# Kernel optimization log

Hardware: AMD Instinct MI355X
Metric: run time of the kernel (lower is better)

Reference implementation:

```python
import jax, jax.numpy as jnp
import numpy as np

B, C, N, T, H = 4, 128, 512, 16, 4
DK = C // H
SCALE = float(np.sqrt(DK) * 1.0)  # dk**0.5 * max(tau,1e-6), tau=1.0


def setup_inputs() -> dict:
    key = jax.random.key(0)
    ks = jax.random.split(key, 6)
    x = jax.random.normal(ks[0], (B, C, N, T), jnp.float32)
    Wq = jax.random.normal(ks[1], (C, C), jnp.float32) * (1.0 / np.sqrt(C))
    Wk = jax.random.normal(ks[2], (C, C), jnp.float32) * (1.0 / np.sqrt(C))
    # original init is identity; add tiny noise so it's not degenerate
    structural = jnp.eye(N, dtype=jnp.float32) + 0.01 * jax.random.normal(ks[3], (N, N), jnp.float32)
    fusion_w = jax.random.normal(ks[4], (2,), jnp.float32) * 0.5  # 1x1 conv over 2 input channels
    fusion_b = (jax.random.normal(ks[5], (), jnp.float32) * 0.1)
    return {"x": x, "Wq": Wq, "Wk": Wk, "structural": structural,
            "fusion_w": fusion_w, "fusion_b": fusion_b}


def reference(x, Wq, Wk, structural, fusion_w, fusion_b):
    # x: [B, C, N, T]. 1x1 conv == per-channel linear; arrange to [B,T,N,H,DK]
    Q = jnp.einsum('oc,bcnt->btno', Wq, x).reshape(B, T, N, H, DK)
    K = jnp.einsum('oc,bcnt->btno', Wk, x).reshape(B, T, N, H, DK)
    # scores: [B, T, H, N, N]
    scores = jnp.einsum('btnhd,btmhd->bthnm', Q, K) / SCALE
    att_node = jax.nn.softmax(scores, axis=-1).mean(axis=(1, 2))  # [B, N, N]
    att_struct = jax.nn.softmax(structural, axis=-1)              # [N, N]
    # fusion conv (1x1, 2->1 channels) == weighted sum + bias
    fused = fusion_w[0] * att_node + fusion_w[1] * att_struct[None] + fusion_b
    fused = 0.5 * (fused + jnp.swapaxes(fused, 1, 2))  # symmetrize
    fused = jax.nn.softmax(fused, axis=-1)             # normalize='softmax'
    x_bt = jnp.transpose(x, (0, 3, 2, 1))              # [B, T, N, C]
    x_att = jnp.einsum('bij,btjc->btic', fused, x_bt)  # weighted aggregation over nodes
    return jnp.transpose(x_att, (0, 3, 2, 1))          # [B, C, N, T]
```

## Files before the change

### kernel.cpp

```cpp
#include <hip/hip_runtime.h>

#define BB 4
#define CC 128
#define NN 512
#define TT 16
#define HH 4
#define DKK 32
#define GPART 8
#define INV_SCALE 0.17677669529663687f

typedef __attribute__((ext_vector_type(8))) short bf16x8;
typedef __attribute__((ext_vector_type(4))) float f32x4;

__device__ __forceinline__ unsigned int pk2bf(float a, float b) {
  unsigned int ua = __float_as_uint(a);
  ua = (ua + 0x7FFFu + ((ua >> 16) & 1u)) >> 16;
  unsigned int ub = __float_as_uint(b);
  ub = (ub + 0x7FFFu + ((ub >> 16) & 1u)) >> 16;
  return ua | (ub << 16);
}

__device__ __forceinline__ ushort cv1(float f) {
  unsigned int u = __float_as_uint(f);
  return (ushort)((u + 0x7FFFu + ((u >> 16) & 1u)) >> 16);
}

__device__ __forceinline__ unsigned int pkfast(float a, float b) {
  unsigned int au = __float_as_uint(a) + 0x8000u;
  unsigned int bu = __float_as_uint(b) + 0x8000u;
  return __builtin_amdgcn_perm(bu, au, 0x07060302u);
}

__device__ __forceinline__ float bf2f(ushort v) {
  return __uint_as_float((unsigned int)v << 16);
}

__global__ __launch_bounds__(256) void k_proj(const float* __restrict__ x,
                                              const float* __restrict__ Wq,
                                              const float* __restrict__ Wk,
                                              ushort* __restrict__ Qb,
                                              ushort* __restrict__ Kb) {
  __shared__ float xl[128 * 66];
  const int b = blockIdx.y;
  const int nt0 = blockIdx.x * 64;
  const int nq = nt0 >> 4;
  const int tid = threadIdx.x;
  const int w = tid >> 6, lane = tid & 63;
  const int lm = lane & 15, quad = lane >> 4;

  const float* xb = x + (size_t)b * 1048576 + nt0;
#pragma unroll
  for (int L = tid * 4; L < 8192; L += 1024) {
    int c = L >> 6, j = L & 63;
    float4 v = *(const float4*)(xb + c * 8192 + j);
    float2* dp = (float2*)(xl + c * 66 + j);
    dp[0] = make_float2(v.x, v.y);
    dp[1] = make_float2(v.z, v.w);
  }

  const int o0 = w * 32;
  bf16x8 aq[2][4], ak[2][4];
#pragma unroll
  for (int ot = 0; ot < 2; ++ot)
#pragma unroll
    for (int kc = 0; kc < 4; ++kc) {
      const int off = (o0 + ot * 16 + lm) * 128 + kc * 32 + quad * 8;
      const float4 q1 = *(const float4*)(Wq + off);
      const float4 q2 = *(const float4*)(Wq + off + 4);
      const float4 k1 = *(const float4*)(Wk + off);
      const float4 k2 = *(const float4*)(Wk + off + 4);
      union { uint4 u; bf16x8 v; } cq, ck;
      cq.u.x = pk2bf(q1.x * INV_SCALE, q1.y * INV_SCALE);
      cq.u.y = pk2bf(q1.z * INV_SCALE, q1.w * INV_SCALE);
      cq.u.z = pk2bf(q2.x * INV_SCALE, q2.y * INV_SCALE);
      cq.u.w = pk2bf(q2.z * INV_SCALE, q2.w * INV_SCALE);
      ck.u.x = pk2bf(k1.x, k1.y);
      ck.u.y = pk2bf(k1.z, k1.w);
      ck.u.z = pk2bf(k2.x, k2.y);
      ck.u.w = pk2bf(k2.z, k2.w);
      aq[ot][kc] = cq.v;
      ak[ot][kc] = ck.v;
    }
  __syncthreads();

#pragma unroll
  for (int jtl = 0; jtl < 4; ++jtl) {
    bf16x8 bfr[4];
#pragma unroll
    for (int kc = 0; kc < 4; ++kc) {
      const float* sp = xl + (kc * 32 + quad * 8) * 66 + jtl * 16 + lm;
      float f0 = sp[0],   f1 = sp[66],  f2 = sp[132], f3 = sp[198];
      float f4 = sp[264], f5 = sp[330], f6 = sp[396], f7 = sp[462];
      union { uint4 u; bf16x8 v; } cv;
      cv.u.x = pkfast(f0, f1);
      cv.u.y = pkfast(f2, f3);
      cv.u.z = pkfast(f4, f5);
      cv.u.w = pkfast(f6, f7);
      bfr[kc] = cv.v;
    }

    f32x4 accq0 = {0,0,0,0}, accq1 = {0,0,0,0};
    f32x4 acck0 = {0,0,0,0}, acck1 = {0,0,0,0};
#pragma unroll
    for (int kc = 0; kc < 4; ++kc) {
      accq0 = __builtin_amdgcn_mfma_f32_16x16x32_bf16(aq[0][kc], bfr[kc], accq0, 0, 0, 0);
      accq1 = __builtin_amdgcn_mfma_f32_16x16x32_bf16(aq[1][kc], bfr[kc], accq1, 0, 0, 0);
      acck0 = __builtin_amdgcn_mfma_f32_16x16x32_bf16(ak[0][kc], bfr[kc], acck0, 0, 0, 0);
      acck1 = __builtin_amdgcn_mfma_f32_16x16x32_bf16(ak[1][kc], bfr[kc], acck1, 0, 0, 0);
    }

    const size_t base = (size_t)b * 1048576 + (size_t)lm * 65536 + w * 16384 +
                        (size_t)(nq + jtl) * 32 + quad * 4;
    uint2 uq0, uq1, uk0, uk1;
    uq0.x = pk2bf(accq0[0], accq0[1]); uq0.y = pk2bf(accq0[2], accq0[3]);
    uq1.x = pk2bf(accq1[0], accq1[1]); uq1.y = pk2bf(accq1[2], accq1[3]);
    uk0.x = pk2bf(acck0[0], acck0[1]); uk0.y = pk2bf(acck0[2], acck0[3]);
    uk1.x = pk2bf(acck1[0], acck1[1]); uk1.y = pk2bf(acck1[2], acck1[3]);
    *(uint2*)(Qb + base)      = uq0;
    *(uint2*)(Qb + base + 16) = uq1;
    *(uint2*)(Kb + base)      = uk0;
    *(uint2*)(Kb + base + 16) = uk1;
  }
}

__global__ __launch_bounds__(256, 4) void k_scores(const ushort* __restrict__ Qb,
                                                   const ushort* __restrict__ Kb,
                                                   ushort* __restrict__ part) {
  __shared__ float SH[16 * 516];
  __shared__ float red[2][4][16];
  const int strip = blockIdx.x, g = blockIdx.y, b = blockIdx.z;
  const int tid = threadIdx.x;
  const int w = tid >> 6, lane = tid & 63;
  const int lm = lane & 15, quad = lane >> 4;
  const int n0 = strip * 16;
  const int wcol0 = w * 128;

  float acc[32];
#pragma unroll
  for (int i = 0; i < 32; ++i) acc[i] = 0.f;

  for (int pi = 0; pi < 8; ++pi) {
    const int p = (g << 3) + pi;
    const size_t base = (size_t)((b * 16 + (p >> 2)) * 4 + (p & 3)) * 16384;
    bf16x8 afrag = *(const bf16x8*)(Qb + base + (size_t)(n0 + lm) * 32 + quad * 8);
    bf16x8 bfr[8];
#pragma unroll
    for (int ct = 0; ct < 8; ++ct)
      bfr[ct] = *(const bf16x8*)(Kb + base + (size_t)(wcol0 + ct * 16 + lm) * 32 + quad * 8);

    f32x4 d[8];
#pragma unroll
    for (int ct = 0; ct < 8; ++ct) {
      f32x4 z = {0.f, 0.f, 0.f, 0.f};
      d[ct] = __builtin_amdgcn_mfma_f32_16x16x32_bf16(afrag, bfr[ct], z, 0, 0, 0);
    }

    float cur[32];
    float rp0 = 0.f, rp1 = 0.f, rp2 = 0.f, rp3 = 0.f;
#pragma unroll
    for (int ct = 0; ct < 8; ++ct) {
      float e0 = __expf(d[ct][0]);
      float e1 = __expf(d[ct][1]);
      float e2 = __expf(d[ct][2]);
      float e3 = __expf(d[ct][3]);
      cur[ct * 4 + 0] = e0; cur[ct * 4 + 1] = e1;
      cur[ct * 4 + 2] = e2; cur[ct * 4 + 3] = e3;
      rp0 += e0; rp1 += e1; rp2 += e2; rp3 += e3;
    }
#pragma unroll
    for (int m = 1; m < 16; m <<= 1) {
      rp0 += __shfl_xor(rp0, m);
      rp1 += __shfl_xor(rp1, m);
      rp2 += __shfl_xor(rp2, m);
      rp3 += __shfl_xor(rp3, m);
    }
    if (lm == 0) {
      red[pi & 1][w][quad * 4 + 0] = rp0;
      red[pi & 1][w][quad * 4 + 1] = rp1;
      red[pi & 1][w][quad * 4 + 2] = rp2;
      red[pi & 1][w][quad * 4 + 3] = rp3;
    }
    __syncthreads();
#pragma unroll
    for (int r = 0; r < 4; ++r) {
      float rs = red[pi & 1][0][quad * 4 + r] + red[pi & 1][1][quad * 4 + r] +
                 red[pi & 1][2][quad * 4 + r] + red[pi & 1][3][quad * 4 + r];
      float inv = 1.0f / rs;
#pragma unroll
      for (int ct = 0; ct < 8; ++ct)
        acc[ct * 4 + r] = fmaf(cur[ct * 4 + r], inv, acc[ct * 4 + r]);
    }
  }

#pragma unroll
  for (int ct = 0; ct < 8; ++ct) {
#pragma unroll
    for (int r = 0; r < 4; ++r)
      SH[(quad * 4 + r) * 516 + wcol0 + ct * 16 + lm] = acc[ct * 4 + r];
  }
  __syncthreads();
  const int row = tid >> 4, colb = (tid & 15) * 4;
  ushort* po = part + ((size_t)((g * 4 + b) * 512 + n0 + row)) * 512 + colb;
#pragma unroll
  for (int k = 0; k < 8; ++k) {
    f32x4 v = *(const f32x4*)(SH + row * 516 + colb + k * 64);
    uint2 u;
    u.x = pk2bf(v[0], v[1]);
    u.y = pk2bf(v[2], v[3]);
    *(uint2*)(po + k * 64) = u;
  }
}

__global__ __launch_bounds__(256) void k_xconv(const float* __restrict__ x,
                                               ushort* __restrict__ xtb) {
  __shared__ ushort xs[16 * 520];
  const int c = blockIdx.x, b = blockIdx.y;
  const int tid = threadIdx.x;
  const float* in = x + ((size_t)b * 128 + c) * 8192;
  ushort* outp = xtb + ((size_t)b * 128 + c) * 8192;

#pragma unroll
  for (int it = 0; it < 8; ++it) {
    int idx = (tid + it * 256) * 4;
    int j = idx >> 4, t0 = idx & 15;
    float4 v = *(const float4*)(in + idx);
    xs[(t0 + 0) * 520 + j] = cv1(v.x);
    xs[(t0 + 1) * 520 + j] = cv1(v.y);
    xs[(t0 + 2) * 520 + j] = cv1(v.z);
    xs[(t0 + 3) * 520 + j] = cv1(v.w);
  }
  __syncthreads();
#pragma unroll
  for (int it = 0; it < 4; ++it) {
    int u = (tid + it * 256) * 8;
    int t = u >> 9, j0 = u & 511;
    *(uint4*)(outp + u) = *(const uint4*)(xs + t * 520 + j0);
  }
}

__device__ __forceinline__ float blk_max(float v, float* red, int tid) {
#pragma unroll
  for (int off = 32; off > 0; off >>= 1) v = fmaxf(v, __shfl_xor(v, off, 64));
  if ((tid & 63) == 0) red[tid >> 6] = v;
  __syncthreads();
  v = fmaxf(fmaxf(red[0], red[1]), fmaxf(red[2], red[3]));
  __syncthreads();
  return v;
}
__device__ __forceinline__ float blk_sum(float v, float* red, int tid) {
#pragma unroll
  for (int off = 32; off > 0; off >>= 1) v += __shfl_xor(v, off, 64);
  if ((tid & 63) == 0) red[tid >> 6] = v;
  __syncthreads();
  v = (red[0] + red[1]) + (red[2] + red[3]);
  __syncthreads();
  return v;
}

__global__ __launch_bounds__(256) void k_struct(const float* __restrict__ S,
                                                float* __restrict__ st) {
  __shared__ float red[4];
  const int i = blockIdx.x, tid = threadIdx.x;
  float s0 = S[i * 512 + tid], s1 = S[i * 512 + tid + 256];
  float m = blk_max(fmaxf(s0, s1), red, tid);
  float e0 = __expf(s0 - m), e1 = __expf(s1 - m);
  float sum = blk_sum(e0 + e1, red, tid);
  float inv = 1.0f / sum;
  st[i * 512 + tid] = e0 * inv;
  st[i * 512 + tid + 256] = e1 * inv;
}

__global__ __launch_bounds__(256) void k_redsym(const ushort* __restrict__ part,
                                                float* __restrict__ Ssym,
                                                float* __restrict__ st) {
  __shared__ float L1[64 * 68];
  __shared__ float L2[64 * 68];
  const int z = blockIdx.y;
  int rem = blockIdx.x, ti = 0;
  for (;;) { int cnt = 8 - ti; if (rem < cnt) break; rem -= cnt; ++ti; }
  const int tj = ti + rem;
  const bool diag = (ti == tj);
  const int tid = threadIdx.x;
  const int rr = tid >> 2, cc = (tid & 3) * 16;

  float a1[16], a2[16];
#pragma unroll
  for (int k = 0; k < 16; ++k) { a1[k] = 0.f; a2[k] = 0.f; }

  if (z == 4) {
    const float* p1 = st + (ti * 64 + rr) * 512 + tj * 64 + cc;
    const float* p2 = st + (tj * 64 + rr) * 512 + ti * 64 + cc;
#pragma unroll
    for (int q = 0; q < 4; ++q) {
      float4 v = *(const float4*)(p1 + q * 4);
      a1[q * 4 + 0] = v.x; a1[q * 4 + 1] = v.y;
      a1[q * 4 + 2] = v.z; a1[q * 4 + 3] = v.w;
      if (!diag) {
        float4 u = *(const float4*)(p2 + q * 4);
        a2[q * 4 + 0] = u.x; a2[q * 4 + 1] = u.y;
        a2[q * 4 + 2] = u.z; a2[q * 4 + 3] = u.w;
      }
    }
  } else {
    const int b = z;
#pragma unroll
    for (int g = 0; g < GPART; ++g) {
      const ushort* p1 = part + ((size_t)((g * 4 + b) * 512 + ti * 64 + rr)) * 512 + tj * 64 + cc;
      const ushort* p2 = part + ((size_t)((g * 4 + b) * 512 + tj * 64 + rr)) * 512 + ti * 64 + cc;
#pragma unroll
      for (int q = 0; q < 4; ++q) {
        ushort4 v = *(const ushort4*)(p1 + q * 4);
        a1[q * 4 + 0] += bf2f(v.x); a1[q * 4 + 1] += bf2f(v.y);
        a1[q * 4 + 2] += bf2f(v.z); a1[q * 4 + 3] += bf2f(v.w);
        if (!diag) {
          ushort4 u = *(const ushort4*)(p2 + q * 4);
          a2[q * 4 + 0] += bf2f(u.x); a2[q * 4 + 1] += bf2f(u.y);
          a2[q * 4 + 2] += bf2f(u.z); a2[q * 4 + 3] += bf2f(u.w);
        }
      }
    }
  }

#pragma unroll
  for (int q = 0; q < 4; ++q) {
    *(float4*)(L1 + rr * 68 + cc + q * 4) =
        make_float4(a1[q * 4], a1[q * 4 + 1], a1[q * 4 + 2], a1[q * 4 + 3]);
    if (!diag)
      *(float4*)(L2 + rr * 68 + cc + q * 4) =
          make_float4(a2[q * 4], a2[q * 4 + 1], a2[q * 4 + 2], a2[q * 4 + 3]);
  }
  __syncthreads();

  float* M = (z < 4) ? (Ssym + (size_t)z * 262144) : st;
  const float* LT = diag ? L1 : L2;
#pragma unroll
  for (int q = 0; q < 4; ++q) {
    const int c = cc + q * 4;
    float4 o;
    o.x = L1[rr * 68 + c + 0] + LT[(c + 0) * 68 + rr];
    o.y = L1[rr * 68 + c + 1] + LT[(c + 1) * 68 + rr];
    o.z = L1[rr * 68 + c + 2] + LT[(c + 2) * 68 + rr];
    o.w = L1[rr * 68 + c + 3] + LT[(c + 3) * 68 + rr];
    *(float4*)(M + (ti * 64 + rr) * 512 + tj * 64 + c) = o;
  }
  if (!diag) {
#pragma unroll
    for (int q = 0; q < 4; ++q) {
      const int c = cc + q * 4;
      float4 o;
      o.x = L2[rr * 68 + c + 0] + L1[(c + 0) * 68 + rr];
      o.y = L2[rr * 68 + c + 1] + L1[(c + 1) * 68 + rr];
      o.z = L2[rr * 68 + c + 2] + L1[(c + 2) * 68 + rr];
      o.w = L2[rr * 68 + c + 3] + L1[(c + 3) * 68 + rr];
      *(float4*)(M + (tj * 64 + rr) * 512 + ti * 64 + c) = o;
    }
  }
}

__global__ __launch_bounds__(256) void k_fused(const float* __restrict__ Ssym,
                                               const float* __restrict__ st,
                                               const float* __restrict__ fw,
                                               const float* __restrict__ fb,
                                               ushort* __restrict__ fusedb) {
  __shared__ float red[4];
  const int i = blockIdx.x, b = blockIdx.y, tid = threadIdx.x;
  const float w0s = fw[0] * (0.5f / 64.f);
  const float w1s = fw[1] * 0.5f;
  const float bias = fb[0];
  const float* A = Ssym + (size_t)b * 262144 + (size_t)i * 512;
  const float* S = st + (size_t)i * 512;
  float2 a2 = *(const float2*)(A + tid * 2);
  float2 s2 = *(const float2*)(S + tid * 2);
  float l0 = fmaf(w0s, a2.x, fmaf(w1s, s2.x, bias));
  float l1 = fmaf(w0s, a2.y, fmaf(w1s, s2.y, bias));
  float m = blk_max(fmaxf(l0, l1), red, tid);
  float e0 = __expf(l0 - m), e1 = __expf(l1 - m);
  float sum = blk_sum(e0 + e1, red, tid);
  float inv = 1.0f / sum;
  *(unsigned int*)(fusedb + ((size_t)(b * 512 + i)) * 512 + tid * 2) =
      pk2bf(e0 * inv, e1 * inv);
}

__global__ __launch_bounds__(256) void k_agg(const ushort* __restrict__ fusedb,
                                             const ushort* __restrict__ xtb,
                                             float* __restrict__ out) {
  __shared__ ushort xs[16 * 520];
  const int cg = blockIdx.x;
  const int i0 = blockIdx.y * 64;
  const int b = blockIdx.z;
  const int tid = threadIdx.x, w = tid >> 6, lane = tid & 63;
  const int lm = lane & 15, quad = lane >> 4;

  const ushort* fr = fusedb + ((size_t)(b * 512 + i0 + w * 16 + lm)) * 512 + quad * 8;
  bf16x8 af[16];
#pragma unroll
  for (int kk = 0; kk < 16; ++kk) af[kk] = *(const bf16x8*)(fr + kk * 32);

  const ushort* xg = xtb + ((size_t)b * 128 + cg * 8) * 8192;
  uint4 rg[4];
#pragma unroll
  for (int it = 0; it < 4; ++it) rg[it] = *(const uint4*)(xg + (tid + it * 256) * 8);

  for (int c = 0; c < 8; ++c) {
#pragma unroll
    for (int it = 0; it < 4; ++it) {
      int u = (tid + it * 256) * 8;
      int t = u >> 9, j0 = u & 511;
      *(uint4*)(xs + t * 520 + j0) = rg[it];
    }
    __syncthreads();
    if (c < 7) {
      const ushort* xg2 = xg + (size_t)(c + 1) * 8192;
#pragma unroll
      for (int it = 0; it < 4; ++it) rg[it] = *(const uint4*)(xg2 + (tid + it * 256) * 8);
    }
    f32x4 acc = {0.f, 0.f, 0.f, 0.f};
#pragma unroll
    for (int kk = 0; kk < 16; ++kk) {
      bf16x8 bf = *(const bf16x8*)(xs + lm * 520 + kk * 32 + quad * 8);
      acc = __builtin_amdgcn_mfma_f32_16x16x32_bf16(af[kk], bf, acc, 0, 0, 0);
    }
    float* op = out + (size_t)b * 1048576 + (size_t)(cg * 8 + c) * 8192 +
                (size_t)(i0 + w * 16 + quad * 4) * 16 + lm;
    op[0]  = acc[0];
    op[16] = acc[1];
    op[32] = acc[2];
    op[48] = acc[3];
    __syncthreads();
  }
}

extern "C" void kernel_launch(void* const* d_in, const int* in_sizes, int n_in,
                              void* d_out, int out_size, void* d_ws, size_t ws_size,
                              hipStream_t stream) {
  const float* x  = (const float*)d_in[0];
  const float* Wq = (const float*)d_in[1];
  const float* Wk = (const float*)d_in[2];
  const float* S  = (const float*)d_in[3];
  const float* fw = (const float*)d_in[4];
  const float* fb = (const float*)d_in[5];
  float* out = (float*)d_out;

  ushort* Qb   = (ushort*)d_ws;
  ushort* Kb   = Qb + 4194304;
  ushort* part = Kb + 4194304;
  ushort* xtb  = part;
  float* Ssym  = (float*)(part + 8388608);
  float* st    = Ssym + 1048576;
  ushort* fusedb = (ushort*)(st + 262144);

  k_proj  <<<dim3(128, 4),      256, 0, stream>>>(x, Wq, Wk, Qb, Kb);
  k_scores<<<dim3(32, GPART, 4),256, 0, stream>>>(Qb, Kb, part);
  k_struct<<<dim3(512),         256, 0, stream>>>(S, st);
  k_redsym<<<dim3(36, 5),       256, 0, stream>>>(part, Ssym, st);
  k_xconv <<<dim3(128, 4),      256, 0, stream>>>(x, xtb);
  k_fused <<<dim3(512, 4),      256, 0, stream>>>(Ssym, st, fw, fb, fusedb);
  k_agg   <<<dim3(16, 8, 4),    256, 0, stream>>>(fusedb, xtb, out);
}
```

Before: 166.6 us.

## Fuse all stages into one cooperative persistent kernel with grid syncs

```diff
diff --git a/kernel.cpp b/kernel.cpp
--- a/kernel.cpp
+++ b/kernel.cpp
@@ -1,13 +1,11 @@
 #include <hip/hip_runtime.h>
-
-#define BB 4
-#define CC 128
-#define NN 512
-#define TT 16
-#define HH 4
-#define DKK 32
-#define GPART 8
+#include <hip/hip_cooperative_groups.h>
+
+namespace cg = cooperative_groups;
+
+#define GPART 4
 #define INV_SCALE 0.17677669529663687f
+#define SMEM_SZ 36864
 
 typedef __attribute__((ext_vector_type(8))) short bf16x8;
 typedef __attribute__((ext_vector_type(4))) float f32x4;
@@ -19,30 +17,24 @@
   ub = (ub + 0x7FFFu + ((ub >> 16) & 1u)) >> 16;
   return ua | (ub << 16);
 }
-
 __device__ __forceinline__ ushort cv1(float f) {
   unsigned int u = __float_as_uint(f);
   return (ushort)((u + 0x7FFFu + ((u >> 16) & 1u)) >> 16);
 }
-
 __device__ __forceinline__ unsigned int pkfast(float a, float b) {
   unsigned int au = __float_as_uint(a) + 0x8000u;
   unsigned int bu = __float_as_uint(b) + 0x8000u;
   return __builtin_amdgcn_perm(bu, au, 0x07060302u);
 }
-
 __device__ __forceinline__ float bf2f(ushort v) {
   return __uint_as_float((unsigned int)v << 16);
 }
 
-__global__ __launch_bounds__(256) void k_proj(const float* __restrict__ x,
-                                              const float* __restrict__ Wq,
-                                              const float* __restrict__ Wk,
-                                              ushort* __restrict__ Qb,
-                                              ushort* __restrict__ Kb) {
-  __shared__ float xl[128 * 66];
-  const int b = blockIdx.y;
-  const int nt0 = blockIdx.x * 64;
+__device__ void ph_proj(const float* x, const float* Wq, const float* Wk,
+                        ushort* Qb, ushort* Kb, char* smem, int bid) {
+  float* xl = (float*)smem;
+  const int b = bid >> 7;
+  const int nt0 = (bid & 127) * 64;
   const int nq = nt0 >> 4;
   const int tid = threadIdx.x;
   const int w = tid >> 6, lane = tid & 63;
@@ -123,12 +115,42 @@
   }
 }
 
-__global__ __launch_bounds__(256, 4) void k_scores(const ushort* __restrict__ Qb,
-                                                   const ushort* __restrict__ Kb,
-                                                   ushort* __restrict__ part) {
-  __shared__ float SH[16 * 516];
-  __shared__ float red[2][4][16];
-  const int strip = blockIdx.x, g = blockIdx.y, b = blockIdx.z;
+__device__ __forceinline__ float blk_max(float v, float* red, int tid) {
+#pragma unroll
+  for (int off = 32; off > 0; off >>= 1) v = fmaxf(v, __shfl_xor(v, off, 64));
+  if ((tid & 63) == 0) red[tid >> 6] = v;
+  __syncthreads();
+  v = fmaxf(fmaxf(red[0], red[1]), fmaxf(red[2], red[3]));
+  __syncthreads();
+  return v;
+}
+__device__ __forceinline__ float blk_sum(float v, float* red, int tid) {
+#pragma unroll
+  for (int off = 32; off > 0; off >>= 1) v += __shfl_xor(v, off, 64);
+  if ((tid & 63) == 0) red[tid >> 6] = v;
+  __syncthreads();
+  v = (red[0] + red[1]) + (red[2] + red[3]);
+  __syncthreads();
+  return v;
+}
+
+__device__ void ph_struct(const float* S, float* st, char* smem, int bid) {
+  float* red = (float*)(smem + 34816);
+  const int i = bid, tid = threadIdx.x;
+  float s0 = S[i * 512 + tid], s1 = S[i * 512 + tid + 256];
+  float m = blk_max(fmaxf(s0, s1), red, tid);
+  float e0 = __expf(s0 - m), e1 = __expf(s1 - m);
+  float sum = blk_sum(e0 + e1, red, tid);
+  float inv = 1.0f / sum;
+  st[i * 512 + tid] = e0 * inv;
+  st[i * 512 + tid + 256] = e1 * inv;
+}
+
+__device__ void ph_scores(const ushort* Qb, const ushort* Kb, ushort* part,
+                          char* smem, int bid) {
+  float* SH = (float*)smem;
+  float (*red)[4][16] = (float(*)[4][16])(smem + 33024);
+  const int strip = bid & 31, g = (bid >> 5) & 3, b = bid >> 7;
   const int tid = threadIdx.x;
   const int w = tid >> 6, lane = tid & 63;
   const int lm = lane & 15, quad = lane >> 4;
@@ -139,8 +161,8 @@
 #pragma unroll
   for (int i = 0; i < 32; ++i) acc[i] = 0.f;
 
-  for (int pi = 0; pi < 8; ++pi) {
-    const int p = (g << 3) + pi;
+  for (int pi = 0; pi < 16; ++pi) {
+    const int p = g * 16 + pi;
     const size_t base = (size_t)((b * 16 + (p >> 2)) * 4 + (p & 3)) * 16384;
     bf16x8 afrag = *(const bf16x8*)(Qb + base + (size_t)(n0 + lm) * 32 + quad * 8);
     bf16x8 bfr[8];
@@ -211,10 +233,9 @@
   }
 }
 
-__global__ __launch_bounds__(256) void k_xconv(const float* __restrict__ x,
-                                               ushort* __restrict__ xtb) {
-  __shared__ ushort xs[16 * 520];
-  const int c = blockIdx.x, b = blockIdx.y;
+__device__ void ph_xconv(const float* x, ushort* xtb, char* smem, int bid) {
+  ushort* xs = (ushort*)smem;
+  const int c = bid & 127, b = bid >> 7;
   const int tid = threadIdx.x;
   const float* in = x + ((size_t)b * 128 + c) * 8192;
   ushort* outp = xtb + ((size_t)b * 128 + c) * 8192;
@@ -238,45 +259,12 @@
   }
 }
 
-__device__ __forceinline__ float blk_max(float v, float* red, int tid) {
-#pragma unroll
-  for (int off = 32; off > 0; off >>= 1) v = fmaxf(v, __shfl_xor(v, off, 64));
-  if ((tid & 63) == 0) red[tid >> 6] = v;
-  __syncthreads();
-  v = fmaxf(fmaxf(red[0], red[1]), fmaxf(red[2], red[3]));
-  __syncthreads();
-  return v;
-}
-__device__ __forceinline__ float blk_sum(float v, float* red, int tid) {
-#pragma unroll
-  for (int off = 32; off > 0; off >>= 1) v += __shfl_xor(v, off, 64);
-  if ((tid & 63) == 0) red[tid >> 6] = v;
-  __syncthreads();
-  v = (red[0] + red[1]) + (red[2] + red[3]);
-  __syncthreads();
-  return v;
-}
-
-__global__ __launch_bounds__(256) void k_struct(const float* __restrict__ S,
-                                                float* __restrict__ st) {
-  __shared__ float red[4];
-  const int i = blockIdx.x, tid = threadIdx.x;
-  float s0 = S[i * 512 + tid], s1 = S[i * 512 + tid + 256];
-  float m = blk_max(fmaxf(s0, s1), red, tid);
-  float e0 = __expf(s0 - m), e1 = __expf(s1 - m);
-  float sum = blk_sum(e0 + e1, red, tid);
-  float inv = 1.0f / sum;
-  st[i * 512 + tid] = e0 * inv;
-  st[i * 512 + tid + 256] = e1 * inv;
-}
-
-__global__ __launch_bounds__(256) void k_redsym(const ushort* __restrict__ part,
-                                                float* __restrict__ Ssym,
-                                                float* __restrict__ st) {
-  __shared__ float L1[64 * 68];
-  __shared__ float L2[64 * 68];
-  const int z = blockIdx.y;
-  int rem = blockIdx.x, ti = 0;
+__device__ void ph_redsym(const ushort* part, float* Ssym, float* st,
+                          char* smem, int bid) {
+  float* L1 = (float*)smem;
+  float* L2 = L1 + 64 * 68;
+  const int z = bid / 36;
+  int rem = bid % 36, ti = 0;
   for (;;) { int cnt = 8 - ti; if (rem < cnt) break; rem -= cnt; ++ti; }
   const int tj = ti + rem;
   const bool diag = (ti == tj);
@@ -357,37 +345,35 @@
   }
 }
 
-__global__ __launch_bounds__(256) void k_fused(const float* __restrict__ Ssym,
-                                               const float* __restrict__ st,
-                                               const float* __restrict__ fw,
-                                               const float* __restrict__ fb,
-                                               ushort* __restrict__ fusedb) {
-  __shared__ float red[4];
-  const int i = blockIdx.x, b = blockIdx.y, tid = threadIdx.x;
+__device__ void ph_fused(const float* Ssym, const float* st, const float* fw,
+                         const float* fb, ushort* fusedb, char* smem, int bid) {
+  float* red = (float*)smem;
+  const int i = bid, tid = threadIdx.x;
   const float w0s = fw[0] * (0.5f / 64.f);
   const float w1s = fw[1] * 0.5f;
   const float bias = fb[0];
-  const float* A = Ssym + (size_t)b * 262144 + (size_t)i * 512;
   const float* S = st + (size_t)i * 512;
-  float2 a2 = *(const float2*)(A + tid * 2);
   float2 s2 = *(const float2*)(S + tid * 2);
-  float l0 = fmaf(w0s, a2.x, fmaf(w1s, s2.x, bias));
-  float l1 = fmaf(w0s, a2.y, fmaf(w1s, s2.y, bias));
-  float m = blk_max(fmaxf(l0, l1), red, tid);
-  float e0 = __expf(l0 - m), e1 = __expf(l1 - m);
-  float sum = blk_sum(e0 + e1, red, tid);
-  float inv = 1.0f / sum;
-  *(unsigned int*)(fusedb + ((size_t)(b * 512 + i)) * 512 + tid * 2) =
-      pk2bf(e0 * inv, e1 * inv);
-}
-
-__global__ __launch_bounds__(256) void k_agg(const ushort* __restrict__ fusedb,
-                                             const ushort* __restrict__ xtb,
-                                             float* __restrict__ out) {
-  __shared__ ushort xs[16 * 520];
-  const int cg = blockIdx.x;
-  const int i0 = blockIdx.y * 64;
-  const int b = blockIdx.z;
+  for (int b = 0; b < 4; ++b) {
+    const float* A = Ssym + (size_t)b * 262144 + (size_t)i * 512;
+    float2 a2 = *(const float2*)(A + tid * 2);
+    float l0 = fmaf(w0s, a2.x, fmaf(w1s, s2.x, bias));
+    float l1 = fmaf(w0s, a2.y, fmaf(w1s, s2.y, bias));
+    float m = blk_max(fmaxf(l0, l1), red, tid);
+    float e0 = __expf(l0 - m), e1 = __expf(l1 - m);
+    float sum = blk_sum(e0 + e1, red, tid);
+    float inv = 1.0f / sum;
+    *(unsigned int*)(fusedb + ((size_t)(b * 512 + i)) * 512 + tid * 2) =
+        pk2bf(e0 * inv, e1 * inv);
+  }
+}
+
+__device__ void ph_agg(const ushort* fusedb, const ushort* xtb, float* out,
+                       char* smem, int bid) {
+  ushort* xs = (ushort*)smem;
+  const int cg = bid & 15;
+  const int i0 = ((bid >> 4) & 7) * 64;
+  const int b = bid >> 7;
   const int tid = threadIdx.x, w = tid >> 6, lane = tid & 63;
   const int lm = lane & 15, quad = lane >> 4;
 
@@ -428,6 +414,63 @@
     op[48] = acc[3];
     __syncthreads();
   }
+}
+
+__global__ __launch_bounds__(256, 2) void k_mega(const float* x, const float* Wq,
+                                                 const float* Wk, const float* S,
+                                                 const float* fw, const float* fb,
+                                                 float* out, ushort* Qb, ushort* Kb,
+                                                 ushort* part, ushort* xtb,
+                                                 float* Ssym, float* st,
+                                                 ushort* fusedb) {
+  __shared__ __align__(16) char smem[SMEM_SZ];
+  const int bid = blockIdx.x;
+  cg::grid_group grid = cg::this_grid();
+
+  ph_proj(x, Wq, Wk, Qb, Kb, smem, bid);
+  ph_struct(S, st, smem, bid);
+  grid.sync();
+  ph_scores(Qb, Kb, part, smem, bid);
+  grid.sync();
+  ph_xconv(x, xtb, smem, bid);
+  __syncthreads();
+  if (bid < 180) ph_redsym(part, Ssym, st, smem, bid);
+  grid.sync();
+  ph_fused(Ssym, st, fw, fb, fusedb, smem, bid);
+  grid.sync();
+  ph_agg(fusedb, xtb, out, smem, bid);
+}
+
+__global__ __launch_bounds__(256, 2) void k_ph1(const float* x, const float* Wq,
+                                                const float* Wk, const float* S,
+                                                ushort* Qb, ushort* Kb, float* st) {
+  __shared__ __align__(16) char smem[SMEM_SZ];
+  ph_proj(x, Wq, Wk, Qb, Kb, smem, blockIdx.x);
+  ph_struct(S, st, smem, blockIdx.x);
+}
+__global__ __launch_bounds__(256, 2) void k_ph2(const ushort* Qb, const ushort* Kb,
+                                                ushort* part) {
+  __shared__ __align__(16) char smem[SMEM_SZ];
+  ph_scores(Qb, Kb, part, smem, blockIdx.x);
+}
+__global__ __launch_bounds__(256, 2) void k_ph3(const float* x, ushort* xtb,
+                                                const ushort* part, float* Ssym,
+                                                float* st) {
+  __shared__ __align__(16) char smem[SMEM_SZ];
+  ph_xconv(x, xtb, smem, blockIdx.x);
+  __syncthreads();
+  if (blockIdx.x < 180) ph_redsym(part, Ssym, st, smem, blockIdx.x);
+}
+__global__ __launch_bounds__(256, 2) void k_ph4(const float* Ssym, const float* st,
+                                                const float* fw, const float* fb,
+                                                ushort* fusedb) {
+  __shared__ __align__(16) char smem[SMEM_SZ];
+  ph_fused(Ssym, st, fw, fb, fusedb, smem, blockIdx.x);
+}
+__global__ __launch_bounds__(256, 2) void k_ph5(const ushort* fusedb,
+                                                const ushort* xtb, float* out) {
+  __shared__ __align__(16) char smem[SMEM_SZ];
+  ph_agg(fusedb, xtb, out, smem, blockIdx.x);
 }
 
 extern "C" void kernel_launch(void* const* d_in, const int* in_sizes, int n_in,
@@ -444,16 +487,21 @@
   ushort* Qb   = (ushort*)d_ws;
   ushort* Kb   = Qb + 4194304;
   ushort* part = Kb + 4194304;
-  ushort* xtb  = part;
-  float* Ssym  = (float*)(part + 8388608);
+  ushort* xtb  = Qb;
+  float* Ssym  = (float*)(part + 4194304);
   float* st    = Ssym + 1048576;
   ushort* fusedb = (ushort*)(st + 262144);
 
-  k_proj  <<<dim3(128, 4),      256, 0, stream>>>(x, Wq, Wk, Qb, Kb);
-  k_scores<<<dim3(32, GPART, 4),256, 0, stream>>>(Qb, Kb, part);
-  k_struct<<<dim3(512),         256, 0, stream>>>(S, st);
-  k_redsym<<<dim3(36, 5),       256, 0, stream>>>(part, Ssym, st);
-  k_xconv <<<dim3(128, 4),      256, 0, stream>>>(x, xtb);
-  k_fused <<<dim3(512, 4),      256, 0, stream>>>(Ssym, st, fw, fb, fusedb);
-  k_agg   <<<dim3(16, 8, 4),    256, 0, stream>>>(fusedb, xtb, out);
-}
+  void* args[] = {(void*)&x, (void*)&Wq, (void*)&Wk, (void*)&S, (void*)&fw,
+                  (void*)&fb, (void*)&out, (void*)&Qb, (void*)&Kb, (void*)&part,
+                  (void*)&xtb, (void*)&Ssym, (void*)&st, (void*)&fusedb};
+  hipError_t e = hipLaunchCooperativeKernel((const void*)k_mega, dim3(512),
+                                            dim3(256), args, 0, stream);
+  if (e != hipSuccess) {
+    k_ph1<<<dim3(512), 256, 0, stream>>>(x, Wq, Wk, S, Qb, Kb, st);
+    k_ph2<<<dim3(512), 256, 0, stream>>>(Qb, Kb, part);
+    k_ph3<<<dim3(512), 256, 0, stream>>>(x, xtb, part, Ssym, st);
+    k_ph4<<<dim3(512), 256, 0, stream>>>(Ssym, st, fw, fb, fusedb);
+    k_ph5<<<dim3(512), 256, 0, stream>>>(fusedb, xtb, out);
+  }
+}
```

Measured after the change: 424.0 us. 154% more time.

## Merge seven kernel launches into five by co-scheduling independent phases

Applied to the files above, without the earlier changes.

```diff
diff --git a/kernel.cpp b/kernel.cpp
--- a/kernel.cpp
+++ b/kernel.cpp
@@ -1,13 +1,8 @@
 #include <hip/hip_runtime.h>
 
-#define BB 4
-#define CC 128
-#define NN 512
-#define TT 16
-#define HH 4
-#define DKK 32
 #define GPART 8
 #define INV_SCALE 0.17677669529663687f
+#define SMEM_SZ 36864
 
 typedef __attribute__((ext_vector_type(8))) short bf16x8;
 typedef __attribute__((ext_vector_type(4))) float f32x4;
@@ -19,30 +14,50 @@
   ub = (ub + 0x7FFFu + ((ub >> 16) & 1u)) >> 16;
   return ua | (ub << 16);
 }
-
 __device__ __forceinline__ ushort cv1(float f) {
   unsigned int u = __float_as_uint(f);
   return (ushort)((u + 0x7FFFu + ((u >> 16) & 1u)) >> 16);
 }
-
 __device__ __forceinline__ unsigned int pkfast(float a, float b) {
   unsigned int au = __float_as_uint(a) + 0x8000u;
   unsigned int bu = __float_as_uint(b) + 0x8000u;
   return __builtin_amdgcn_perm(bu, au, 0x07060302u);
 }
-
 __device__ __forceinline__ float bf2f(ushort v) {
   return __uint_as_float((unsigned int)v << 16);
 }
 
-__global__ __launch_bounds__(256) void k_proj(const float* __restrict__ x,
-                                              const float* __restrict__ Wq,
-                                              const float* __restrict__ Wk,
-                                              ushort* __restrict__ Qb,
-                                              ushort* __restrict__ Kb) {
-  __shared__ float xl[128 * 66];
-  const int b = blockIdx.y;
-  const int nt0 = blockIdx.x * 64;
+__device__ __forceinline__ float blk_max(float v, float* red, int tid) {
+#pragma unroll
+  for (int off = 32; off > 0; off >>= 1) v = fmaxf(v, __shfl_xor(v, off, 64));
+  if ((tid & 63) == 0) red[tid >> 6] = v;
+  __syncthreads();
+  v = fmaxf(fmaxf(red[0], red[1]), fmaxf(red[2], red[3]));
+  __syncthreads();
+  return v;
+}
+__device__ __forceinline__ float blk_sum(float v, float* red, int tid) {
+#pragma unroll
+  for (int off = 32; off > 0; off >>= 1) v += __shfl_xor(v, off, 64);
+  if ((tid & 63) == 0) red[tid >> 6] = v;
+  __syncthreads();
+  v = (red[0] + red[1]) + (red[2] + red[3]);
+  __syncthreads();
+  return v;
+}
+
+__global__ __launch_bounds__(256) void k_ph1(const float* __restrict__ x,
+                                             const float* __restrict__ Wq,
+                                             const float* __restrict__ Wk,
+                                             const float* __restrict__ S,
+                                             ushort* __restrict__ Qb,
+                                             ushort* __restrict__ Kb,
+                                             float* __restrict__ st) {
+  __shared__ __align__(16) char smem[SMEM_SZ];
+  float* xl = (float*)smem;
+  const int bid = blockIdx.x;
+  const int b = bid >> 7;
+  const int nt0 = (bid & 127) * 64;
   const int nq = nt0 >> 4;
   const int tid = threadIdx.x;
   const int w = tid >> 6, lane = tid & 63;
@@ -121,11 +136,24 @@
     *(uint2*)(Kb + base)      = uk0;
     *(uint2*)(Kb + base + 16) = uk1;
   }
-}
-
-__global__ __launch_bounds__(256, 4) void k_scores(const ushort* __restrict__ Qb,
-                                                   const ushort* __restrict__ Kb,
-                                                   ushort* __restrict__ part) {
+
+  {
+    float* red = (float*)(smem + 34816);
+    __syncthreads();
+    const int i = bid;
+    float s0 = S[i * 512 + tid], s1 = S[i * 512 + tid + 256];
+    float m = blk_max(fmaxf(s0, s1), red, tid);
+    float e0 = __expf(s0 - m), e1 = __expf(s1 - m);
+    float sum = blk_sum(e0 + e1, red, tid);
+    float inv = 1.0f / sum;
+    st[i * 512 + tid] = e0 * inv;
+    st[i * 512 + tid + 256] = e1 * inv;
+  }
+}
+
+__global__ __launch_bounds__(256, 4) void k_ph2(const ushort* __restrict__ Qb,
+                                                const ushort* __restrict__ Kb,
+                                                ushort* __restrict__ part) {
   __shared__ float SH[16 * 516];
   __shared__ float red[2][4][16];
   const int strip = blockIdx.x, g = blockIdx.y, b = blockIdx.z;
@@ -211,177 +239,151 @@
   }
 }
 
-__global__ __launch_bounds__(256) void k_xconv(const float* __restrict__ x,
-                                               ushort* __restrict__ xtb) {
-  __shared__ ushort xs[16 * 520];
-  const int c = blockIdx.x, b = blockIdx.y;
+__global__ __launch_bounds__(256) void k_ph3(const float* __restrict__ x,
+                                             ushort* __restrict__ xtb,
+                                             const ushort* __restrict__ part,
+                                             float* __restrict__ Ssym,
+                                             float* __restrict__ st) {
+  __shared__ __align__(16) char smem[SMEM_SZ];
+  const int bid = blockIdx.x;
   const int tid = threadIdx.x;
-  const float* in = x + ((size_t)b * 128 + c) * 8192;
-  ushort* outp = xtb + ((size_t)b * 128 + c) * 8192;
-
-#pragma unroll
-  for (int it = 0; it < 8; ++it) {
-    int idx = (tid + it * 256) * 4;
-    int j = idx >> 4, t0 = idx & 15;
-    float4 v = *(const float4*)(in + idx);
-    xs[(t0 + 0) * 520 + j] = cv1(v.x);
-    xs[(t0 + 1) * 520 + j] = cv1(v.y);
-    xs[(t0 + 2) * 520 + j] = cv1(v.z);
-    xs[(t0 + 3) * 520 + j] = cv1(v.w);
-  }
-  __syncthreads();
-#pragma unroll
-  for (int it = 0; it < 4; ++it) {
-    int u = (tid + it * 256) * 8;
-    int t = u >> 9, j0 = u & 511;
-    *(uint4*)(outp + u) = *(const uint4*)(xs + t * 520 + j0);
-  }
-}
-
-__device__ __forceinline__ float blk_max(float v, float* red, int tid) {
-#pragma unroll
-  for (int off = 32; off > 0; off >>= 1) v = fmaxf(v, __shfl_xor(v, off, 64));
-  if ((tid & 63) == 0) red[tid >> 6] = v;
-  __syncthreads();
-  v = fmaxf(fmaxf(red[0], red[1]), fmaxf(red[2], red[3]));
-  __syncthreads();
-  return v;
-}
-__device__ __forceinline__ float blk_sum(float v, float* red, int tid) {
-#pragma unroll
-  for (int off = 32; off > 0; off >>= 1) v += __shfl_xor(v, off, 64);
-  if ((tid & 63) == 0) red[tid >> 6] = v;
-  __syncthreads();
-  v = (red[0] + red[1]) + (red[2] + red[3]);
-  __syncthreads();
-  return v;
-}
-
-__global__ __launch_bounds__(256) void k_struct(const float* __restrict__ S,
-                                                float* __restrict__ st) {
-  __shared__ float red[4];
-  const int i = blockIdx.x, tid = threadIdx.x;
-  float s0 = S[i * 512 + tid], s1 = S[i * 512 + tid + 256];
-  float m = blk_max(fmaxf(s0, s1), red, tid);
-  float e0 = __expf(s0 - m), e1 = __expf(s1 - m);
-  float sum = blk_sum(e0 + e1, red, tid);
-  float inv = 1.0f / sum;
-  st[i * 512 + tid] = e0 * inv;
-  st[i * 512 + tid + 256] = e1 * inv;
-}
-
-__global__ __launch_bounds__(256) void k_redsym(const ushort* __restrict__ part,
-                                                float* __restrict__ Ssym,
-                                                float* __restrict__ st) {
-  __shared__ float L1[64 * 68];
-  __shared__ float L2[64 * 68];
-  const int z = blockIdx.y;
-  int rem = blockIdx.x, ti = 0;
-  for (;;) { int cnt = 8 - ti; if (rem < cnt) break; rem -= cnt; ++ti; }
-  const int tj = ti + rem;
-  const bool diag = (ti == tj);
-  const int tid = threadIdx.x;
-  const int rr = tid >> 2, cc = (tid & 3) * 16;
-
-  float a1[16], a2[16];
-#pragma unroll
-  for (int k = 0; k < 16; ++k) { a1[k] = 0.f; a2[k] = 0.f; }
-
-  if (z == 4) {
-    const float* p1 = st + (ti * 64 + rr) * 512 + tj * 64 + cc;
-    const float* p2 = st + (tj * 64 + rr) * 512 + ti * 64 + cc;
-#pragma unroll
-    for (int q = 0; q < 4; ++q) {
-      float4 v = *(const float4*)(p1 + q * 4);
-      a1[q * 4 + 0] = v.x; a1[q * 4 + 1] = v.y;
-      a1[q * 4 + 2] = v.z; a1[q * 4 + 3] = v.w;
-      if (!diag) {
-        float4 u = *(const float4*)(p2 + q * 4);
-        a2[q * 4 + 0] = u.x; a2[q * 4 + 1] = u.y;
-        a2[q * 4 + 2] = u.z; a2[q * 4 + 3] = u.w;
-      }
-    }
-  } else {
-    const int b = z;
-#pragma unroll
-    for (int g = 0; g < GPART; ++g) {
-      const ushort* p1 = part + ((size_t)((g * 4 + b) * 512 + ti * 64 + rr)) * 512 + tj * 64 + cc;
-      const ushort* p2 = part + ((size_t)((g * 4 + b) * 512 + tj * 64 + rr)) * 512 + ti * 64 + cc;
+
+  {
+    ushort* xs = (ushort*)smem;
+    const int c = bid & 127, b = bid >> 7;
+    const float* in = x + ((size_t)b * 128 + c) * 8192;
+    ushort* outp = xtb + ((size_t)b * 128 + c) * 8192;
+#pragma unroll
+    for (int it = 0; it < 8; ++it) {
+      int idx = (tid + it * 256) * 4;
+      int j = idx >> 4, t0 = idx & 15;
+      float4 v = *(const float4*)(in + idx);
+      xs[(t0 + 0) * 520 + j] = cv1(v.x);
+      xs[(t0 + 1) * 520 + j] = cv1(v.y);
+      xs[(t0 + 2) * 520 + j] = cv1(v.z);
+      xs[(t0 + 3) * 520 + j] = cv1(v.w);
+    }
+    __syncthreads();
+#pragma unroll
+    for (int it = 0; it < 4; ++it) {
+      int u = (tid + it * 256) * 8;
+      int t = u >> 9, j0 = u & 511;
+      *(uint4*)(outp + u) = *(const uint4*)(xs + t * 520 + j0);
+    }
+  }
+  __syncthreads();
+
+  if (bid < 180) {
+    float* L1 = (float*)smem;
+    float* L2 = L1 + 64 * 68;
+    const int z = bid / 36;
+    int rem = bid % 36, ti = 0;
+    for (;;) { int cnt = 8 - ti; if (rem < cnt) break; rem -= cnt; ++ti; }
+    const int tj = ti + rem;
+    const bool diag = (ti == tj);
+    const int rr = tid >> 2, cc = (tid & 3) * 16;
+
+    float a1[16], a2[16];
+#pragma unroll
+    for (int k = 0; k < 16; ++k) { a1[k] = 0.f; a2[k] = 0.f; }
+
+    if (z == 4) {
+      const float* p1 = st + (ti * 64 + rr) * 512 + tj * 64 + cc;
+      const float* p2 = st + (tj * 64 + rr) * 512 + ti * 64 + cc;
 #pragma unroll
       for (int q = 0; q < 4; ++q) {
-        ushort4 v = *(const ushort4*)(p1 + q * 4);
-        a1[q * 4 + 0] += bf2f(v.x); a1[q * 4 + 1] += bf2f(v.y);
-        a1[q * 4 + 2] += bf2f(v.z); a1[q * 4 + 3] += bf2f(v.w);
+        float4 v = *(const float4*)(p1 + q * 4);
+        a1[q * 4 + 0] = v.x; a1[q * 4 + 1] = v.y;
+        a1[q * 4 + 2] = v.z; a1[q * 4 + 3] = v.w;
         if (!diag) {
-          ushort4 u = *(const ushort4*)(p2 + q * 4);
-          a2[q * 4 + 0] += bf2f(u.x); a2[q * 4 + 1] += bf2f(u.y);
-          a2[q * 4 + 2] += bf2f(u.z); a2[q * 4 + 3] += bf2f(u.w);
+          float4 u = *(const float4*)(p2 + q * 4);
+          a2[q * 4 + 0] = u.x; a2[q * 4 + 1] = u.y;
+          a2[q * 4 + 2] = u.z; a2[q * 4 + 3] = u.w;
         }
       }
-    }
-  }
-
-#pragma unroll
-  for (int q = 0; q < 4; ++q) {
-    *(float4*)(L1 + rr * 68 + cc + q * 4) =
-        make_float4(a1[q * 4], a1[q * 4 + 1], a1[q * 4 + 2], a1[q * 4 + 3]);
-    if (!diag)
-      *(float4*)(L2 + rr * 68 + cc + q * 4) =
-          make_float4(a2[q * 4], a2[q * 4 + 1], a2[q * 4 + 2], a2[q * 4 + 3]);
-  }
-  __syncthreads();
-
-  float* M = (z < 4) ? (Ssym + (size_t)z * 262144) : st;
-  const float* LT = diag ? L1 : L2;
-#pragma unroll
-  for (int q = 0; q < 4; ++q) {
-    const int c = cc + q * 4;
-    float4 o;
-    o.x = L1[rr * 68 + c + 0] + LT[(c + 0) * 68 + rr];
-    o.y = L1[rr * 68 + c + 1] + LT[(c + 1) * 68 + rr];
-    o.z = L1[rr * 68 + c + 2] + LT[(c + 2) * 68 + rr];
-    o.w = L1[rr * 68 + c + 3] + LT[(c + 3) * 68 + rr];
-    *(float4*)(M + (ti * 64 + rr) * 512 + tj * 64 + c) = o;
-  }
-  if (!diag) {
+    } else {
+      const int b = z;
+#pragma unroll
+      for (int g = 0; g < GPART; ++g) {
+        const ushort* p1 = part + ((size_t)((g * 4 + b) * 512 + ti * 64 + rr)) * 512 + tj * 64 + cc;
+        const ushort* p2 = part + ((size_t)((g * 4 + b) * 512 + tj * 64 + rr)) * 512 + ti * 64 + cc;
+#pragma unroll
+        for (int q = 0; q < 4; ++q) {
+          ushort4 v = *(const ushort4*)(p1 + q * 4);
+          a1[q * 4 + 0] += bf2f(v.x); a1[q * 4 + 1] += bf2f(v.y);
+          a1[q * 4 + 2] += bf2f(v.z); a1[q * 4 + 3] += bf2f(v.w);
+          if (!diag) {
+            ushort4 u = *(const ushort4*)(p2 + q * 4);
+            a2[q * 4 + 0] += bf2f(u.x); a2[q * 4 + 1] += bf2f(u.y);
+            a2[q * 4 + 2] += bf2f(u.z); a2[q * 4 + 3] += bf2f(u.w);
+          }
+        }
+      }
+    }
+
+#pragma unroll
+    for (int q = 0; q < 4; ++q) {
+      *(float4*)(L1 + rr * 68 + cc + q * 4) =
+          make_float4(a1[q * 4], a1[q * 4 + 1], a1[q * 4 + 2], a1[q * 4 + 3]);
+      if (!diag)
+        *(float4*)(L2 + rr * 68 + cc + q * 4) =
+            make_float4(a2[q * 4], a2[q * 4 + 1], a2[q * 4 + 2], a2[q * 4 + 3]);
+    }
+    __syncthreads();
+
+    float* M = (z < 4) ? (Ssym + (size_t)z * 262144) : st;
+    const float* LT = diag ? L1 : L2;
 #pragma unroll
     for (int q = 0; q < 4; ++q) {
       const int c = cc + q * 4;
       float4 o;
-      o.x = L2[rr * 68 + c + 0] + L1[(c + 0) * 68 + rr];
-      o.y = L2[rr * 68 + c + 1] + L1[(c + 1) * 68 + rr];
-      o.z = L2[rr * 68 + c + 2] + L1[(c + 2) * 68 + rr];
-      o.w = L2[rr * 68 + c + 3] + L1[(c + 3) * 68 + rr];
-      *(float4*)(M + (tj * 64 + rr) * 512 + ti * 64 + c) = o;
-    }
-  }
-}
-
-__global__ __launch_bounds__(256) void k_fused(const float* __restrict__ Ssym,
-                                               const float* __restrict__ st,
-                                               const float* __restrict__ fw,
-                                               const float* __restrict__ fb,
-                                               ushort* __restrict__ fusedb) {
+      o.x = L1[rr * 68 + c + 0] + LT[(c + 0) * 68 + rr];
+      o.y = L1[rr * 68 + c + 1] + LT[(c + 1) * 68 + rr];
+      o.z = L1[rr * 68 + c + 2] + LT[(c + 2) * 68 + rr];
+      o.w = L1[rr * 68 + c + 3] + LT[(c + 3) * 68 + rr];
+      *(float4*)(M + (ti * 64 + rr) * 512 + tj * 64 + c) = o;
+    }
+    if (!diag) {
+#pragma unroll
+      for (int q = 0; q < 4; ++q) {
+        const int c = cc + q * 4;
+        float4 o;
+        o.x = L2[rr * 68 + c + 0] + L1[(c + 0) * 68 + rr];
+        o.y = L2[rr * 68 + c + 1] + L1[(c + 1) * 68 + rr];
+        o.z = L2[rr * 68 + c + 2] + L1[(c + 2) * 68 + rr];
+        o.w = L2[rr * 68 + c + 3] + L1[(c + 3) * 68 + rr];
+        *(float4*)(M + (tj * 64 + rr) * 512 + ti * 64 + c) = o;
+      }
+    }
+  }
+}
+
+__global__ __launch_bounds__(256) void k_ph4(const float* __restrict__ Ssym,
+                                             const float* __restrict__ st,
+                                             const float* __restrict__ fw,
+                                             const float* __restrict__ fb,
+                                             ushort* __restrict__ fusedb) {
   __shared__ float red[4];
-  const int i = blockIdx.x, b = blockIdx.y, tid = threadIdx.x;
+  const int i = blockIdx.x, tid = threadIdx.x;
   const float w0s = fw[0] * (0.5f / 64.f);
   const float w1s = fw[1] * 0.5f;
   const float bias = fb[0];
-  const float* A = Ssym + (size_t)b * 262144 + (size_t)i * 512;
-  const float* S = st + (size_t)i * 512;
-  float2 a2 = *(const float2*)(A + tid * 2);
-  float2 s2 = *(const float2*)(S + tid * 2);
-  float l0 = fmaf(w0s, a2.x, fmaf(w1s, s2.x, bias));
-  float l1 = fmaf(w0s, a2.y, fmaf(w1s, s2.y, bias));
-  float m = blk_max(fmaxf(l0, l1), red, tid);
-  float e0 = __expf(l0 - m), e1 = __expf(l1 - m);
-  float sum = blk_sum(e0 + e1, red, tid);
-  float inv = 1.0f / sum;
-  *(unsigned int*)(fusedb + ((size_t)(b * 512 + i)) * 512 + tid * 2) =
-      pk2bf(e0 * inv, e1 * inv);
-}
-
-__global__ __launch_bounds__(256) void k_agg(const ushort* __restrict__ fusedb,
+  float2 s2 = *(const float2*)(st + (size_t)i * 512 + tid * 2);
+  for (int b = 0; b < 4; ++b) {
+    const float* A = Ssym + (size_t)b * 262144 + (size_t)i * 512;
+    float2 a2 = *(const float2*)(A + tid * 2);
+    float l0 = fmaf(w0s, a2.x, fmaf(w1s, s2.x, bias));
+    float l1 = fmaf(w0s, a2.y, fmaf(w1s, s2.y, bias));
+    float m = blk_max(fmaxf(l0, l1), red, tid);
+    float e0 = __expf(l0 - m), e1 = __expf(l1 - m);
+    float sum = blk_sum(e0 + e1, red, tid);
+    float inv = 1.0f / sum;
+    *(unsigned int*)(fusedb + ((size_t)(b * 512 + i)) * 512 + tid * 2) =
+        pk2bf(e0 * inv, e1 * inv);
+  }
+}
+
+__global__ __launch_bounds__(256) void k_ph5(const ushort* __restrict__ fusedb,
                                              const ushort* __restrict__ xtb,
                                              float* __restrict__ out) {
   __shared__ ushort xs[16 * 520];
@@ -444,16 +446,14 @@
   ushort* Qb   = (ushort*)d_ws;
   ushort* Kb   = Qb + 4194304;
   ushort* part = Kb + 4194304;
-  ushort* xtb  = part;
+  ushort* xtb  = Qb;
   float* Ssym  = (float*)(part + 8388608);
   float* st    = Ssym + 1048576;
   ushort* fusedb = (ushort*)(st + 262144);
 
-  k_proj  <<<dim3(128, 4),      256, 0, stream>>>(x, Wq, Wk, Qb, Kb);
-  k_scores<<<dim3(32, GPART, 4),256, 0, stream>>>(Qb, Kb, part);
-  k_struct<<<dim3(512),         256, 0, stream>>>(S, st);
-  k_redsym<<<dim3(36, 5),       256, 0, stream>>>(part, Ssym, st);
-  k_xconv <<<dim3(128, 4),      256, 0, stream>>>(x, xtb);
-  k_fused <<<dim3(512, 4),      256, 0, stream>>>(Ssym, st, fw, fb, fusedb);
-  k_agg   <<<dim3(16, 8, 4),    256, 0, stream>>>(fusedb, xtb, out);
-}
+  k_ph1<<<dim3(512),          256, 0, stream>>>(x, Wq, Wk, S, Qb, Kb, st);
+  k_ph2<<<dim3(32, GPART, 4), 256, 0, stream>>>(Qb, Kb, part);
+  k_ph3<<<dim3(512),          256, 0, stream>>>(x, xtb, part, Ssym, st);
+  k_ph4<<<dim3(512),          256, 0, stream>>>(Ssym, st, fw, fb, fusedb);
+  k_ph5<<<dim3(16, 8, 4),     256, 0, stream>>>(fusedb, xtb, out);
+}
```

After: 163.6 us. Within noise of the previous version (-1.8%).
